# Kernel tuning notes

Hardware: AMD Instinct MI355X
Metric: run time of the kernel (lower is better)

## Reference

```python
import jax, jax.numpy as jnp
import numpy as np

B, N, CIN, H, D, K = 8, 1000, 16, 64, 16, 3  # batch, nodes, in_dim, hidden, embed_dim, cheb_k
XIN = CIN + H  # GRU concat input dim


def setup_inputs() -> dict:
    key = jax.random.key(0)
    ks = jax.random.split(key, 18)
    f = lambda k, s, sc=1.0: jax.random.normal(k, s, dtype=jnp.float32) * sc
    inp = {}
    inp['x1'] = f(ks[0], (B, N, CIN)); inp['x2'] = f(ks[1], (B, N, CIN)); inp['x3'] = f(ks[2], (B, N, CIN))
    inp['state1'] = f(ks[3], (B, N, H)); inp['state2'] = f(ks[4], (B, N, H)); inp['state3'] = f(ks[5], (B, N, H))
    for i, name in enumerate(['support1', 'support2', 'support3']):
        a = jax.random.uniform(ks[6 + i], (N, N), dtype=jnp.float32)
        inp[name] = a / a.sum(-1, keepdims=True)  # row-stochastic graph, keeps Chebyshev stable
    inp['embeddings1'] = f(ks[9], (N, D), 0.1); inp['embeddings2'] = f(ks[10], (N, D), 0.1); inp['embeddings3'] = f(ks[11], (N, D), 0.1)
    inp['mode_embedding'] = f(ks[12], (3, D), 0.5)
    # xavier-normal-ish scales for the hypernet weight pools
    inp['Wg'] = f(ks[13], (D, K * XIN, 2 * H), (2.0 / (K * XIN * 2 * H + D * 2 * H)) ** 0.5)
    inp['Bg'] = f(ks[14], (D, 2 * H), (2.0 / (D + 2 * H)) ** 0.5)
    inp['Wu'] = f(ks[15], (D, K * XIN, H), (2.0 / (K * XIN * H + D * H)) ** 0.5)
    inp['Bu'] = f(ks[16], (D, H), (2.0 / (D + H)) ** 0.5)
    return inp


def _cheb_gcn(x, support, emb, wp, bp):
    # x:[B,N,C], support:[N,N], emb:[N,D], wp:[D,K*C,O], bp:[D,O]
    # Chebyshev recurrence applied directly to features (equivalent to building T_k(support))
    terms = [x, jnp.einsum('nm,bmc->bnc', support, x)]
    for _ in range(2, K):
        terms.append(2.0 * jnp.einsum('nm,bmc->bnc', support, terms[-1]) - terms[-2])
    x_g = jnp.concatenate(terms, axis=-1)  # [B,N,K*C]
    # meta_axis='S': per-node weights = emb @ wp ; fused contraction
    out = jnp.einsum('bni,nd,dio->bno', x_g, emb, wp) + emb @ bp  # [B,N,O]
    return out


def _cell(x, state, support, emb, me, Wg, Bg, Wu, Bu):
    # me:[D] mode embedding scales the shared pools (einsum 'mc,cdf->mcdf' -> pick mode m)
    zr = jax.nn.sigmoid(_cheb_gcn(jnp.concatenate([x, state], -1), support, emb,
                                  me[:, None, None] * Wg, me[:, None] * Bg))
    z, r = jnp.split(zr, 2, axis=-1)
    hc = jnp.tanh(_cheb_gcn(jnp.concatenate([x, z * state], -1), support, emb,
                            me[:, None, None] * Wu, me[:, None] * Bu))
    return r * state + (1.0 - r) * hc


def reference(x1, x2, x3, state1, state2, state3, support1, support2, support3,
              embeddings1, embeddings2, embeddings3, mode_embedding, Wg, Bg, Wu, Bu):
    h1 = _cell(x1, state1, support1, embeddings1, mode_embedding[0], Wg, Bg, Wu, Bu)
    h2 = _cell(x2, state2, support2, embeddings2, mode_embedding[1], Wg, Bg, Wu, Bu)
    h3 = _cell(x3, state3, support3, embeddings3, mode_embedding[2], Wg, Bg, Wu, Bu)
    return (h1, h2, h3)
```

## Files before the change

### kernel.cpp

```cpp
#include <hip/hip_runtime.h>
#include <math.h>


typedef __attribute__((ext_vector_type(8))) short s16x8;
typedef __attribute__((ext_vector_type(4))) float f32x4;
typedef unsigned short u16;
typedef unsigned int u32;
typedef unsigned long long u64;

__device__ __forceinline__ u32 f2bf(float f) {
  union { float f; u32 u; } v; v.f = f;
  return (v.u + 0x7FFFu + ((v.u >> 16) & 1u)) >> 16;
}
__device__ __forceinline__ float bf2f(u16 h) {
  union { u32 u; float f; } v; v.u = (u32)h << 16; return v.f;
}
__device__ __forceinline__ u64 pk4(float a, float b, float c, float d) {
  return (u64)f2bf(a) | ((u64)f2bf(b) << 16) | ((u64)f2bf(c) << 32) |
         ((u64)f2bf(d) << 48);
}
__device__ __forceinline__ void glds16(const u16* g, u16* l) {
  __builtin_amdgcn_global_load_lds(
      (const __attribute__((address_space(1))) void*)g,
      (__attribute__((address_space(3))) void*)l, 16, 0, 0);
}

#define E0 3145728
#define E1 1966080
#define E2 1920000
#define E3 384000
#define E4 384000
#define E5 384000
#define E6 119808

struct PrepArgs {
  const float* x[3]; const float* st[3]; const float* S[3];
  u16 *S16, *Xt, *Ag, *AgU, *T1t, *ZSt, *SZ1t;
};

__global__ void prep_v(PrepArgs P) {
  long idx = ((long)blockIdx.x * 256 + threadIdx.x) * 4;
  if (idx < E0) {
    int m = (int)(idx >> 20); int rem = (int)(idx & 1048575);
    int n = rem >> 10, k = rem & 1023;
    u64 pv = 0;
    if (n < 1000 && k < 1000) {
      f32x4 v = *(const f32x4*)&P.S[m][n * 1000 + k];
      pv = pk4(v[0], v[1], v[2], v[3]);
    }
    *(u64*)&P.S16[(size_t)m * 1048576 + rem] = pv; return;
  }
  idx -= E0;
  if (idx < E1) {
    int m = (int)(idx / 655360); int rem = (int)(idx % 655360);
    int col = rem >> 10, nn = rem & 1023;
    int b = col / 80, c = col % 80;
    u64 pv = 0;
    if (nn < 1000) {
      float f[4];
#pragma unroll
      for (int j = 0; j < 4; ++j)
        f[j] = (c < 16) ? P.x[m][(b * 1000 + nn + j) * 16 + c]
                        : P.st[m][(b * 1000 + nn + j) * 64 + c - 16];
      pv = pk4(f[0], f[1], f[2], f[3]);
    }
    *(u64*)&P.Xt[(size_t)m * 655360 + rem] = pv; return;
  }
  idx -= E1;
  if (idx < E2) {
    int m = (int)(idx / 640000); int rem = (int)(idx % 640000);
    int r = rem / 80, c = rem % 80;
    int n = r >> 3, b = r & 7;
    f32x4 v = (c < 16) ? *(const f32x4*)&P.x[m][(b * 1000 + n) * 16 + c]
                       : *(const f32x4*)&P.st[m][(b * 1000 + n) * 64 + c - 16];
    *(u64*)&P.Ag[(size_t)m * 2048000 + (size_t)r * 256 + c] =
        pk4(v[0], v[1], v[2], v[3]);
    return;
  }
  idx -= E2;
  if (idx < E3) {
    int m = (int)(idx / 128000); int rem = (int)(idx % 128000);
    int r = rem / 16, c = 240 + rem % 16;
    *(u64*)&P.Ag[(size_t)m * 2048000 + (size_t)r * 256 + c] = 0; return;
  }
  idx -= E3;
  if (idx < E4) {
    int m = (int)(idx / 128000); int rem = (int)(idx % 128000);
    int r = rem / 16, c = rem % 16;
    int n = r >> 3, b = r & 7;
    f32x4 v = *(const f32x4*)&P.x[m][(b * 1000 + n) * 16 + c];
    *(u64*)&P.AgU[(size_t)m * 2048000 + (size_t)r * 256 + c] =
        pk4(v[0], v[1], v[2], v[3]);
    return;
  }
  idx -= E4;
  if (idx < E5) {
    int m = (int)(idx / 128000); int rem = (int)(idx % 128000);
    int r = rem / 16, c = 240 + rem % 16;
    *(u64*)&P.AgU[(size_t)m * 2048000 + (size_t)r * 256 + c] = 0; return;
  }
  idx -= E5;
  if (idx < E6) {
    int m = (int)(idx / 39936); int rem = (int)(idx % 39936);
    if (rem < 15360) { int col = rem / 24, j = rem % 24;
      *(u64*)&P.T1t[(size_t)m * 655360 + col * 1024 + 1000 + j] = 0; }
    else if (rem < 27648) { int e = rem - 15360; int col = e / 24, j = e % 24;
      *(u64*)&P.ZSt[(size_t)m * 524288 + col * 1024 + 1000 + j] = 0; }
    else { int e = rem - 27648; int col = e / 24, j = e % 24;
      *(u64*)&P.SZ1t[(size_t)m * 524288 + col * 1024 + 1000 + j] = 0; }
    return;
  }
}

__global__ void aux_kernel(const float* __restrict__ e0, const float* __restrict__ e1,
                           const float* __restrict__ e2, const float* __restrict__ me,
                           const float* __restrict__ Bg, const float* __restrict__ Bu,
                           const float* __restrict__ Wg, const float* __restrict__ Wu,
                           float* __restrict__ BiG, float* __restrict__ BiU,
                           u16* __restrict__ BtG, u16* __restrict__ BtU) {
  int idx = blockIdx.x * blockDim.x + threadIdx.x;
  if (idx < 384000) {
    int mode = idx / 128000, rem = idx % 128000;
    int n = rem >> 7, o = rem & 127;
    const float* emb = (mode == 0) ? e0 : (mode == 1) ? e1 : e2;
    float s = 0.f;
#pragma unroll
    for (int d = 0; d < 16; ++d)
      s += emb[n * 16 + d] * me[mode * 16 + d] * Bg[d * 128 + o];
    BiG[idx] = s; return;
  }
  idx -= 384000;
  if (idx < 192000) {
    int mode = idx / 64000, rem = idx % 64000;
    int n = rem >> 6, o = rem & 63;
    const float* emb = (mode == 0) ? e0 : (mode == 1) ? e1 : e2;
    float s = 0.f;
#pragma unroll
    for (int d = 0; d < 16; ++d)
      s += emb[n * 16 + d] * me[mode * 16 + d] * Bu[d * 64 + o];
    BiU[idx] = s; return;
  }
  idx -= 192000;
  if (idx < 524288) {
    int col = idx >> 8, k = idx & 255;
    int d = col >> 7, o = col & 127;
    BtG[idx] = (k < 240) ? (u16)f2bf(Wg[d * 30720 + k * 128 + o]) : (u16)0;
    return;
  }
  idx -= 524288;
  {
    int col = idx >> 8, k = idx & 255;
    int d = col >> 6, o = col & 63;
    BtU[idx] = (k < 240) ? (u16)f2bf(Wu[d * 15360 + k * 64 + o]) : (u16)0;
  }
}

struct ChebArgs2 {
  const u16* S16[3]; const u16* A[3]; const u16* Res[3];
  u16* Yt[3]; u16* AgA[3]; u16* AgX[3];
};

__global__ __launch_bounds__(256, 2) void cheb_v4(ChebArgs2 g, int fdiv, int agbase,
                                                  float alpha, float beta, int flags) {
  const int mode = blockIdx.z;
  const u16* __restrict__ Ab = g.A[mode];
  const u16* __restrict__ Sb = g.S16[mode];

  __shared__ u16 As[64 * 64];
  __shared__ u16 Bs[64 * 64];

  const int t = threadIdx.x;
  const int row0 = blockIdx.y * 64, n0 = blockIdx.x * 64;
  const int lane = t & 63, wid = t >> 6;
  const int l16 = lane & 15, quad = lane >> 4;
  const int wy = (wid >> 1) * 32, wx = (wid & 1) * 32;

  f32x4 acc[2][2];
#pragma unroll
  for (int a = 0; a < 2; ++a)
#pragma unroll
    for (int b = 0; b < 2; ++b) acc[a][b] = (f32x4){0.f, 0.f, 0.f, 0.f};

  for (int k0 = 0; k0 < 1024; k0 += 64) {
#pragma unroll
    for (int p = 0; p < 2; ++p) {
      int idx = p * 256 + t; int row = idx >> 3; int cs = (idx & 7) ^ (row & 7);
      glds16(Ab + (size_t)(row0 + row) * 1024 + k0 + cs * 8, &As[idx * 8]);
    }
#pragma unroll
    for (int p = 0; p < 2; ++p) {
      int idx = p * 256 + t; int row = idx >> 3; int cs = (idx & 7) ^ (row & 7);
      glds16(Sb + (size_t)(n0 + row) * 1024 + k0 + cs * 8, &Bs[idx * 8]);
    }
    __syncthreads();
    s16x8 af[2][2], bf[2][2];
#pragma unroll
    for (int mi = 0; mi < 2; ++mi) {
      int row = wy + mi * 16 + l16;
#pragma unroll
      for (int ks = 0; ks < 2; ++ks) {
        int cl = (ks * 4 + quad) ^ (row & 7);
        af[mi][ks] = *(const s16x8*)&As[row * 64 + cl * 8];
      }
    }
#pragma unroll
    for (int ni = 0; ni < 2; ++ni) {
      int row = wx + ni * 16 + l16;
#pragma unroll
      for (int ks = 0; ks < 2; ++ks) {
        int cl = (ks * 4 + quad) ^ (row & 7);
        bf[ni][ks] = *(const s16x8*)&Bs[row * 64 + cl * 8];
      }
    }
#pragma unroll
    for (int ks = 0; ks < 2; ++ks)
#pragma unroll
      for (int mi = 0; mi < 2; ++mi)
#pragma unroll
        for (int ni = 0; ni < 2; ++ni)
          acc[mi][ni] = __builtin_amdgcn_mfma_f32_16x16x32_bf16(af[mi][ks], bf[ni][ks], acc[mi][ni], 0, 0, 0);
    __syncthreads();
  }

#pragma unroll
  for (int mi = 0; mi < 2; ++mi) {
    int frow0 = row0 + wy + mi * 16 + quad * 4;
    int b = frow0 / fdiv, c0 = frow0 - b * fdiv;
#pragma unroll
    for (int ni = 0; ni < 2; ++ni) {
      int n = n0 + wx + ni * 16 + l16;
      if (n < 1000) {
        u16 pk[4];
#pragma unroll
        for (int r = 0; r < 4; ++r) {
          float v = alpha * acc[mi][ni][r];
          if (flags & 1) v += beta * bf2f(g.Res[mode][(size_t)(frow0 + r) * 1024 + n]);
          u16 h = (u16)f2bf(v);
          pk[r] = h;
          if (flags & 2) g.Yt[mode][(size_t)(frow0 + r) * 1024 + n] = h;
        }
        u64 pv = (u64)pk[0] | ((u64)pk[1] << 16) | ((u64)pk[2] << 32) | ((u64)pk[3] << 48);
        *(u64*)&g.AgA[mode][(size_t)(n * 8 + b) * 256 + agbase + c0] = pv;
        if ((flags & 4) && c0 < 16)
          *(u64*)&g.AgX[mode][(size_t)(n * 8 + b) * 256 + agbase + c0] = pv;
      }
    }
  }
}

struct Meta3Args {
  const u16* Ag;
  const u16* Bt;
  const float* emb[3];
  const float* me;
  const float* Bias;
  const float* state[3];
  u16* ZSt;
  u16* AgU;
  float* Rb;
  float* out;
};

__global__ __launch_bounds__(256, 4) void meta3(Meta3Args A, int is_gate, int O) {
  const int mode = blockIdx.z;
  const int row0 = blockIdx.y * 64;
  const int n0 = row0 >> 3;
  const int oc = blockIdx.x;
  const int ocbase = oc * 64;

  __shared__ u16 Bs[64 * 256];
  __shared__ float ewS[8][17];

  const int t = threadIdx.x;
  if (t < 128) {
    int nl = t >> 4, d = t & 15;
    ewS[nl][d] = A.emb[mode][(n0 + nl) * 16 + d] * A.me[mode * 16 + d];
  }

  const int lane = t & 63, wid = t >> 6;
  const int l16 = lane & 15, quad = lane >> 4;
  const int wy = (wid >> 1) * 32, wx = (wid & 1) * 32;
  const u16* Agm = A.Ag + (size_t)mode * 2048000;

#pragma unroll
  for (int p = 0; p < 8; ++p) {
    int idx = p * 256 + t; int row = idx >> 5; int cs = (idx & 31) ^ (row & 7);
    glds16(Agm + (size_t)(row0 + row) * 256 + cs * 8, &Bs[idx * 8]);
  }
  __syncthreads();

  s16x8 afr[2][8];
#pragma unroll
  for (int mi = 0; mi < 2; ++mi) {
    int row = wy + mi * 16 + l16;
#pragma unroll
    for (int ki = 0; ki < 8; ++ki) {
      int cl = (ki * 4 + quad) ^ (row & 7);
      afr[mi][ki] = *(const s16x8*)&Bs[row * 256 + cl * 8];
    }
  }
  __syncthreads();

  f32x4 outacc[2][2];
#pragma unroll
  for (int a = 0; a < 2; ++a)
#pragma unroll
    for (int b = 0; b < 2; ++b) outacc[a][b] = (f32x4){0.f, 0.f, 0.f, 0.f};

  for (int tl = 0; tl < 16; ++tl) {
    const int brow0 = tl * O + ocbase;
#pragma unroll
    for (int p = 0; p < 8; ++p) {
      int idx = p * 256 + t; int row = idx >> 5; int cs = (idx & 31) ^ (row & 7);
      glds16(A.Bt + (size_t)(brow0 + row) * 256 + cs * 8, &Bs[idx * 8]);
    }
    __syncthreads();

    f32x4 acc[2][2];
#pragma unroll
    for (int a = 0; a < 2; ++a)
#pragma unroll
      for (int b = 0; b < 2; ++b) acc[a][b] = (f32x4){0.f, 0.f, 0.f, 0.f};

#pragma unroll
    for (int ki = 0; ki < 8; ++ki) {
      s16x8 bfr[2];
#pragma unroll
      for (int ni = 0; ni < 2; ++ni) {
        int row = wx + ni * 16 + l16;
        int cl = (ki * 4 + quad) ^ (row & 7);
        bfr[ni] = *(const s16x8*)&Bs[row * 256 + cl * 8];
      }
#pragma unroll
      for (int mi = 0; mi < 2; ++mi)
#pragma unroll
        for (int ni = 0; ni < 2; ++ni)
          acc[mi][ni] = __builtin_amdgcn_mfma_f32_16x16x32_bf16(afr[mi][ki], bfr[ni], acc[mi][ni], 0, 0, 0);
    }

#pragma unroll
    for (int mi = 0; mi < 2; ++mi) {
      int nl = (wy + mi * 16 + quad * 4) >> 3;
      float s = ewS[nl][tl];
#pragma unroll
      for (int ni = 0; ni < 2; ++ni)
#pragma unroll
        for (int r = 0; r < 4; ++r)
          outacc[mi][ni][r] += s * acc[mi][ni][r];
    }
    __syncthreads();
  }

#pragma unroll
  for (int mi = 0; mi < 2; ++mi)
#pragma unroll
    for (int ni = 0; ni < 2; ++ni)
#pragma unroll
      for (int r = 0; r < 4; ++r) {
        int row = row0 + wy + mi * 16 + quad * 4 + r;
        int n = row >> 3, b = row & 7;
        int o = ocbase + wx + ni * 16 + l16;
        float pre = outacc[mi][ni][r] + A.Bias[(size_t)mode * 1000 * O + n * O + o];
        if (is_gate) {
          float sg = 1.f / (1.f + __expf(-pre));
          if (o < 64) {
            float st = A.state[mode][(b * 1000 + n) * 64 + o];
            float zs = sg * st;
            A.ZSt[(size_t)mode * 524288 + (size_t)(b * 64 + o) * 1024 + n] = (u16)f2bf(zs);
            A.AgU[(size_t)mode * 2048000 + (size_t)row * 256 + 16 + o] = (u16)f2bf(zs);
          } else {
            A.Rb[(size_t)mode * 512000 + row * 64 + (o - 64)] = sg;
          }
        } else {
          float hc = tanhf(pre);
          float rr = A.Rb[(size_t)mode * 512000 + row * 64 + o];
          float st = A.state[mode][(b * 1000 + n) * 64 + o];
          A.out[(size_t)mode * 512000 + (b * 1000 + n) * 64 + o] = rr * st + (1.f - rr) * hc;
        }
      }
}

extern "C" void kernel_launch(void* const* d_in, const int* in_sizes, int n_in,
                              void* d_out, int out_size, void* d_ws, size_t ws_size,
                              hipStream_t stream) {
  const float* x[3]   = {(const float*)d_in[0], (const float*)d_in[1], (const float*)d_in[2]};
  const float* st[3]  = {(const float*)d_in[3], (const float*)d_in[4], (const float*)d_in[5]};
  const float* S[3]   = {(const float*)d_in[6], (const float*)d_in[7], (const float*)d_in[8]};
  const float* emb[3] = {(const float*)d_in[9], (const float*)d_in[10], (const float*)d_in[11]};
  const float* me = (const float*)d_in[12];
  const float* Wg = (const float*)d_in[13];
  const float* Bg = (const float*)d_in[14];
  const float* Wu = (const float*)d_in[15];
  const float* Bu = (const float*)d_in[16];
  float* out = (float*)d_out;

  float* BiG = (float*)d_ws;
  float* BiU = BiG + 384000;
  float* Rb  = BiU + 192000;
  u16* S16 = (u16*)(Rb + 1536000);
  u16* Xt  = S16 + 3145728;
  u16* T1t = Xt + 1966080;
  u16* ZSt = T1t + 1966080;
  u16* SZ1t= ZSt + 1572864;
  u16* Ag  = SZ1t + 1572864;
  u16* AgU = Ag + 6144000;
  u16* BtG = AgU + 6144000;
  u16* BtU = BtG + 524288;

  {
    PrepArgs P;
    for (int m = 0; m < 3; ++m) { P.x[m] = x[m]; P.st[m] = st[m]; P.S[m] = S[m]; }
    P.S16 = S16; P.Xt = Xt; P.Ag = Ag; P.AgU = AgU; P.T1t = T1t; P.ZSt = ZSt; P.SZ1t = SZ1t;
    prep_v<<<8109, 256, 0, stream>>>(P);
  }
  aux_kernel<<<5322, 256, 0, stream>>>(emb[0], emb[1], emb[2], me, Bg, Bu,
                                       Wg, Wu, BiG, BiU, BtG, BtU);

  {
    ChebArgs2 a;
    for (int m = 0; m < 3; ++m) {
      a.S16[m] = S16 + (size_t)m * 1048576; a.A[m] = Xt + (size_t)m * 655360;
      a.Res[m] = nullptr; a.Yt[m] = T1t + (size_t)m * 655360;
      a.AgA[m] = Ag + (size_t)m * 2048000; a.AgX[m] = AgU + (size_t)m * 2048000;
    }
    cheb_v4<<<dim3(16, 10, 3), 256, 0, stream>>>(a, 80, 80, 1.f, 0.f, 2 | 4);
  }
  {
    ChebArgs2 a;
    for (int m = 0; m < 3; ++m) {
      a.S16[m] = S16 + (size_t)m * 1048576; a.A[m] = T1t + (size_t)m * 655360;
      a.Res[m] = Xt + (size_t)m * 655360; a.Yt[m] = nullptr;
      a.AgA[m] = Ag + (size_t)m * 2048000; a.AgX[m] = AgU + (size_t)m * 2048000;
    }
    cheb_v4<<<dim3(16, 10, 3), 256, 0, stream>>>(a, 80, 160, 2.f, -1.f, 1 | 4);
  }
  {
    Meta3Args a;
    a.Ag = Ag; a.Bt = BtG; a.me = me; a.Bias = BiG;
    a.ZSt = ZSt; a.AgU = AgU; a.Rb = Rb; a.out = out;
    for (int m = 0; m < 3; ++m) { a.emb[m] = emb[m]; a.state[m] = st[m]; }
    meta3<<<dim3(2, 125, 3), 256, 0, stream>>>(a, 1, 128);
  }
  {
    ChebArgs2 a;
    for (int m = 0; m < 3; ++m) {
      a.S16[m] = S16 + (size_t)m * 1048576; a.A[m] = ZSt + (size_t)m * 524288;
      a.Res[m] = nullptr; a.Yt[m] = SZ1t + (size_t)m * 524288;
      a.AgA[m] = AgU + (size_t)m * 2048000; a.AgX[m] = nullptr;
    }
    cheb_v4<<<dim3(16, 8, 3), 256, 0, stream>>>(a, 64, 96, 1.f, 0.f, 2);
  }
  {
    ChebArgs2 a;
    for (int m = 0; m < 3; ++m) {
      a.S16[m] = S16 + (size_t)m * 1048576; a.A[m] = SZ1t + (size_t)m * 524288;
      a.Res[m] = ZSt + (size_t)m * 524288; a.Yt[m] = nullptr;
      a.AgA[m] = AgU + (size_t)m * 2048000; a.AgX[m] = nullptr;
    }
    cheb_v4<<<dim3(16, 8, 3), 256, 0, stream>>>(a, 64, 176, 2.f, -1.f, 1);
  }
  {
    Meta3Args a;
    a.Ag = AgU; a.Bt = BtU; a.me = me; a.Bias = BiU;
    a.ZSt = ZSt; a.AgU = AgU; a.Rb = Rb; a.out = out;
    for (int m = 0; m < 3; ++m) { a.emb[m] = emb[m]; a.state[m] = st[m]; }
    meta3<<<dim3(1, 125, 3), 256, 0, stream>>>(a, 0, 64);
  }
}
```

Baseline: 262.3 us.

## Pre-swizzle weight pool into MFMA fragment order and load B directly to registers

The weight-pool conversion now writes the bf16 weights in the exact per-lane MFMA fragment order, so meta3 can fetch B fragments straight from global memory into registers. This removes the per-tile LDS staging and the block-wide barriers. Each wave now owns a 16-column output strip and covers all 64 rows (4 A fragments kept in registers), and launch bounds drop to 2 blocks per SM. The cost is higher register pressure and uncached global loads of B in every wave. A dummy LDS write/read was also added, apparently to keep the shared buffer alive; launch grid dimensions must match the new per-wave column mapping.

```diff
diff --git a/kernel.cpp b/kernel.cpp
--- a/kernel.cpp
+++ b/kernel.cpp
@@ -142,15 +142,19 @@
   }
   idx -= 192000;
   if (idx < 524288) {
-    int col = idx >> 8, k = idx & 255;
-    int d = col >> 7, o = col & 127;
+    int e = idx & 7, lane = (idx >> 3) & 63, ki = (idx >> 9) & 7;
+    int j = (idx >> 12) & 7, d = idx >> 15;
+    int k = ki * 32 + (lane >> 4) * 8 + e;
+    int o = j * 16 + (lane & 15);
     BtG[idx] = (k < 240) ? (u16)f2bf(Wg[d * 30720 + k * 128 + o]) : (u16)0;
     return;
   }
   idx -= 524288;
   {
-    int col = idx >> 8, k = idx & 255;
-    int d = col >> 6, o = col & 63;
+    int e = idx & 7, lane = (idx >> 3) & 63, ki = (idx >> 9) & 7;
+    int j = (idx >> 12) & 3, d = idx >> 14;
+    int k = ki * 32 + (lane >> 4) * 8 + e;
+    int o = j * 16 + (lane & 15);
     BtU[idx] = (k < 240) ? (u16)f2bf(Wu[d * 15360 + k * 64 + o]) : (u16)0;
   }
 }
@@ -261,14 +265,14 @@
   float* out;
 };
 
-__global__ __launch_bounds__(256, 4) void meta3(Meta3Args A, int is_gate, int O) {
+__global__ __launch_bounds__(256, 2) void meta3(Meta3Args A, int is_gate, int O) {
   const int mode = blockIdx.z;
   const int row0 = blockIdx.y * 64;
   const int n0 = row0 >> 3;
   const int oc = blockIdx.x;
-  const int ocbase = oc * 64;
-
-  __shared__ u16 Bs[64 * 256];
+  const int J = O >> 4;
+
+  __shared__ u16 As[64 * 256];
   __shared__ float ewS[8][17];
 
   const int t = threadIdx.x;
@@ -279,105 +283,89 @@
 
   const int lane = t & 63, wid = t >> 6;
   const int l16 = lane & 15, quad = lane >> 4;
-  const int wy = (wid >> 1) * 32, wx = (wid & 1) * 32;
   const u16* Agm = A.Ag + (size_t)mode * 2048000;
 
 #pragma unroll
   for (int p = 0; p < 8; ++p) {
     int idx = p * 256 + t; int row = idx >> 5; int cs = (idx & 31) ^ (row & 7);
-    glds16(Agm + (size_t)(row0 + row) * 256 + cs * 8, &Bs[idx * 8]);
+    glds16(Agm + (size_t)(row0 + row) * 256 + cs * 8, &As[idx * 8]);
   }
   __syncthreads();
 
-  s16x8 afr[2][8];
-#pragma unroll
-  for (int mi = 0; mi < 2; ++mi) {
-    int row = wy + mi * 16 + l16;
+  s16x8 afr[4][8];
+#pragma unroll
+  for (int mi = 0; mi < 4; ++mi) {
+    int row = mi * 16 + l16;
 #pragma unroll
     for (int ki = 0; ki < 8; ++ki) {
       int cl = (ki * 4 + quad) ^ (row & 7);
-      afr[mi][ki] = *(const s16x8*)&Bs[row * 256 + cl * 8];
+      afr[mi][ki] = *(const s16x8*)&As[row * 256 + cl * 8];
     }
   }
   __syncthreads();
-
-  f32x4 outacc[2][2];
-#pragma unroll
-  for (int a = 0; a < 2; ++a)
-#pragma unroll
-    for (int b = 0; b < 2; ++b) outacc[a][b] = (f32x4){0.f, 0.f, 0.f, 0.f};
+  As[(t * 131) & 16383] = (u16)t;
+  __syncthreads();
+  { u16 rb = As[(t * 67) & 16383]; u32 rv = rb;
+    asm volatile("" :: "v"(rv)); }
+
+  f32x4 outacc[4];
+#pragma unroll
+  for (int a = 0; a < 4; ++a) outacc[a] = (f32x4){0.f, 0.f, 0.f, 0.f};
+
+  const s16x8* __restrict__ Bf = (const s16x8*)A.Bt;
+  const int jw = oc * 4 + wid;
 
   for (int tl = 0; tl < 16; ++tl) {
-    const int brow0 = tl * O + ocbase;
-#pragma unroll
-    for (int p = 0; p < 8; ++p) {
-      int idx = p * 256 + t; int row = idx >> 5; int cs = (idx & 31) ^ (row & 7);
-      glds16(A.Bt + (size_t)(brow0 + row) * 256 + cs * 8, &Bs[idx * 8]);
-    }
-    __syncthreads();
-
-    f32x4 acc[2][2];
-#pragma unroll
-    for (int a = 0; a < 2; ++a)
-#pragma unroll
-      for (int b = 0; b < 2; ++b) acc[a][b] = (f32x4){0.f, 0.f, 0.f, 0.f};
-
-#pragma unroll
-    for (int ki = 0; ki < 8; ++ki) {
-      s16x8 bfr[2];
-#pragma unroll
-      for (int ni = 0; ni < 2; ++ni) {
-        int row = wx + ni * 16 + l16;
-        int cl = (ki * 4 + quad) ^ (row & 7);
-        bfr[ni] = *(const s16x8*)&Bs[row * 256 + cl * 8];
+    s16x8 bfr[8];
+#pragma unroll
+    for (int ki = 0; ki < 8; ++ki)
+      bfr[ki] = Bf[(((tl * J + jw) * 8 + ki) << 6) + lane];
+
+    f32x4 acc[4];
+#pragma unroll
+    for (int a = 0; a < 4; ++a) acc[a] = (f32x4){0.f, 0.f, 0.f, 0.f};
+
+#pragma unroll
+    for (int ki = 0; ki < 8; ++ki)
+#pragma unroll
+      for (int mi = 0; mi < 4; ++mi)
+        acc[mi] = __builtin_amdgcn_mfma_f32_16x16x32_bf16(afr[mi][ki], bfr[ki], acc[mi], 0, 0, 0);
+
+#pragma unroll
+    for (int mi = 0; mi < 4; ++mi) {
+      int nl = (mi * 16 + quad * 4) >> 3;
+      float s = ewS[nl][tl];
+#pragma unroll
+      for (int r = 0; r < 4; ++r)
+        outacc[mi][r] += s * acc[mi][r];
+    }
+  }
+
+  const int o = jw * 16 + l16;
+#pragma unroll
+  for (int mi = 0; mi < 4; ++mi)
+#pragma unroll
+    for (int r = 0; r < 4; ++r) {
+      int row = row0 + mi * 16 + quad * 4 + r;
+      int n = row >> 3, b = row & 7;
+      float pre = outacc[mi][r] + A.Bias[(size_t)mode * 1000 * O + n * O + o];
+      if (is_gate) {
+        float sg = 1.f / (1.f + __expf(-pre));
+        if (o < 64) {
+          float st = A.state[mode][(b * 1000 + n) * 64 + o];
+          float zs = sg * st;
+          A.ZSt[(size_t)mode * 524288 + (size_t)(b * 64 + o) * 1024 + n] = (u16)f2bf(zs);
+          A.AgU[(size_t)mode * 2048000 + (size_t)row * 256 + 16 + o] = (u16)f2bf(zs);
+        } else {
+          A.Rb[(size_t)mode * 512000 + row * 64 + (o - 64)] = sg;
+        }
+      } else {
+        float hc = tanhf(pre);
+        float rr = A.Rb[(size_t)mode * 512000 + row * 64 + o];
+        float st = A.state[mode][(b * 1000 + n) * 64 + o];
+        A.out[(size_t)mode * 512000 + (b * 1000 + n) * 64 + o] = rr * st + (1.f - rr) * hc;
       }
-#pragma unroll
-      for (int mi = 0; mi < 2; ++mi)
-#pragma unroll
-        for (int ni = 0; ni < 2; ++ni)
-          acc[mi][ni] = __builtin_amdgcn_mfma_f32_16x16x32_bf16(afr[mi][ki], bfr[ni], acc[mi][ni], 0, 0, 0);
-    }
-
-#pragma unroll
-    for (int mi = 0; mi < 2; ++mi) {
-      int nl = (wy + mi * 16 + quad * 4) >> 3;
-      float s = ewS[nl][tl];
-#pragma unroll
-      for (int ni = 0; ni < 2; ++ni)
-#pragma unroll
-        for (int r = 0; r < 4; ++r)
-          outacc[mi][ni][r] += s * acc[mi][ni][r];
-    }
-    __syncthreads();
-  }
-
-#pragma unroll
-  for (int mi = 0; mi < 2; ++mi)
-#pragma unroll
-    for (int ni = 0; ni < 2; ++ni)
-#pragma unroll
-      for (int r = 0; r < 4; ++r) {
-        int row = row0 + wy + mi * 16 + quad * 4 + r;
-        int n = row >> 3, b = row & 7;
-        int o = ocbase + wx + ni * 16 + l16;
-        float pre = outacc[mi][ni][r] + A.Bias[(size_t)mode * 1000 * O + n * O + o];
-        if (is_gate) {
-          float sg = 1.f / (1.f + __expf(-pre));
-          if (o < 64) {
-            float st = A.state[mode][(b * 1000 + n) * 64 + o];
-            float zs = sg * st;
-            A.ZSt[(size_t)mode * 524288 + (size_t)(b * 64 + o) * 1024 + n] = (u16)f2bf(zs);
-            A.AgU[(size_t)mode * 2048000 + (size_t)row * 256 + 16 + o] = (u16)f2bf(zs);
-          } else {
-            A.Rb[(size_t)mode * 512000 + row * 64 + (o - 64)] = sg;
-          }
-        } else {
-          float hc = tanhf(pre);
-          float rr = A.Rb[(size_t)mode * 512000 + row * 64 + o];
-          float st = A.state[mode][(b * 1000 + n) * 64 + o];
-          A.out[(size_t)mode * 512000 + (b * 1000 + n) * 64 + o] = rr * st + (1.f - rr) * hc;
-        }
-      }
+    }
 }
 
 extern "C" void kernel_launch(void* const* d_in, const int* in_sizes, int n_in,
```

After: 293.4 us. +11.9%, slower.
